# Optimization experiments

Hardware: AMD Instinct MI355X
Metric: run time of the kernel (lower is better)

## Reference

```python
import jax, jax.numpy as jnp
import numpy as np

NUM_NODES = 2_000_000
NUM_PINS = 8_000_000


def setup_inputs() -> dict:
    key = jax.random.key(0)
    k1, k2, k3 = jax.random.split(key, 3)
    # CSR offsets: sorted, pinned to [0, NUM_PINS]
    starts = jnp.sort(jax.random.randint(k1, (NUM_NODES + 1,), 0, NUM_PINS + 1, dtype=jnp.int32))
    starts = starts.at[0].set(0).at[-1].set(NUM_PINS)
    # flat node->pin map: a permutation of all pin ids (each pin belongs to one node)
    flat_node2pin = jax.random.permutation(k2, NUM_PINS).astype(jnp.int32)
    # per-pin sort key (a permutation -> unique keys, like a global pin ordering)
    sorted_pin_map = jax.random.permutation(k3, NUM_PINS).astype(jnp.int32)
    return {
        "flat_node2pin_start": starts,
        "flat_node2pin": flat_node2pin,
        "sorted_pin_map": sorted_pin_map,
        "num_nodes": NUM_NODES,
    }


def reference(flat_node2pin_start, flat_node2pin, sorted_pin_map, num_nodes):
    """For each node, return the pin id (from its CSR segment) with the minimum
    sorted_pin_map value; 0 for nodes with no pins (matching zeros init)."""
    num_pins = flat_node2pin.shape[0]
    pin_pos = jnp.arange(num_pins, dtype=jnp.int32)
    # segment id for each flat pin slot: node i owns [starts[i], starts[i+1])
    seg = (jnp.searchsorted(flat_node2pin_start, pin_pos, side="right") - 1).astype(jnp.int32)
    key = sorted_pin_map[flat_node2pin]  # ordering key per flat slot
    min_key = jax.ops.segment_min(key, seg, num_segments=num_nodes)  # [num_nodes]
    # pick the pin achieving the min key (ties -> smallest pin id, keys unique here)
    cand = jnp.where(key == min_key[seg], flat_node2pin, jnp.int32(num_pins))
    best_pin = jax.ops.segment_min(cand, seg, num_segments=num_nodes)
    counts = flat_node2pin_start[1:] - flat_node2pin_start[:-1]
    node2pinId = jnp.where(counts > 0, best_pin, jnp.int32(0)).astype(jnp.int32)
    return node2pinId
```

## Files before the change

### kernel.cpp

```cpp
#include <hip/hip_runtime.h>
#include <stdint.h>


typedef int iv4 __attribute__((ext_vector_type(4)));

#define NPB 512
#define NT  256
#define CAP 2560
#define PINMASK 0x7FFFFFu

__global__ void build_key4_kernel(const int* __restrict__ key,
                                  uint32_t* __restrict__ key4,
                                  int num_pins, int shift) {
    int t = blockIdx.x * blockDim.x + threadIdx.x;
    int base = t * 8;
    if (base >= num_pins) return;
    if (base + 8 <= num_pins) {
        const iv4* kp = (const iv4*)(key + base);
        iv4 a = __builtin_nontemporal_load(kp);
        iv4 b = __builtin_nontemporal_load(kp + 1);
        uint32_t w = 0;
        w |= (((uint32_t)a.x >> shift) & 15u) << 0;
        w |= (((uint32_t)a.y >> shift) & 15u) << 4;
        w |= (((uint32_t)a.z >> shift) & 15u) << 8;
        w |= (((uint32_t)a.w >> shift) & 15u) << 12;
        w |= (((uint32_t)b.x >> shift) & 15u) << 16;
        w |= (((uint32_t)b.y >> shift) & 15u) << 20;
        w |= (((uint32_t)b.z >> shift) & 15u) << 24;
        w |= (((uint32_t)b.w >> shift) & 15u) << 28;
        __builtin_nontemporal_store(w, key4 + t);
    } else {
        uint32_t w = 0;
        for (int j = 0; base + j < num_pins; ++j) {
            uint32_t k = (uint32_t)key[base + j];
            w |= ((k >> shift) & 15u) << (4 * j);
        }
        __builtin_nontemporal_store(w, key4 + t);
    }
}

__device__ __forceinline__ uint32_t nib_of(const uint32_t* key4, uint32_t p) {
    uint32_t w = key4[p >> 3];
    return (w >> ((p & 7u) * 4u)) & 15u;
}

__device__ __forceinline__ iv4 load_chunk(const int* __restrict__ n2p,
                                          int jal, int jbeg, int jend, int c) {
    int j0 = jal + (c << 2);
    if (j0 >= jbeg && j0 + 4 <= jend) {
        return __builtin_nontemporal_load((const iv4*)(n2p + j0));
    }
    iv4 r;
    #pragma unroll
    for (int e = 0; e < 4; ++e) {
        int j = j0 + e;
        r[e] = (j >= jbeg && j < jend) ? __builtin_nontemporal_load(n2p + j)
                                       : -1;
    }
    return r;
}

__device__ __forceinline__ uint32_t pack_sv(const uint32_t* key4, int pi) {
    if (pi < 0) return 0xFFFFFFFFu;
    uint32_t p = (uint32_t)pi;
    return (nib_of(key4, p) << 23) | p;
}

__device__ __forceinline__ void upd3(uint32_t sp, uint32_t& m1, uint32_t& m2,
                                     uint32_t& m3) {
    uint32_t a = min(sp, m1);
    uint32_t b = max(sp, m1);
    uint32_t c = min(b, m2);
    uint32_t d = max(b, m2);
    m1 = a; m2 = c; m3 = min(d, m3);
}

__device__ __forceinline__ int scan_seg3(const uint32_t* slot, int s, int e,
                                         const int* __restrict__ key) {
    if (e <= s) return 0;
    uint32_t m1 = ~0u, m2 = ~0u, m3 = ~0u;
    for (int q = (s & ~3); q < e; q += 4) {
        iv4 v = *(const iv4*)(slot + q);
        #pragma unroll
        for (int u = 0; u < 4; ++u) {
            int j = q + u;
            uint32_t sp = (uint32_t)v[u];
            sp = (j >= s && j < e) ? sp : ~0u;
            upd3(sp, m1, m2, m3);
        }
    }
    uint32_t nib1 = m1 >> 23;
    if ((m2 >> 23) != nib1) return (int)(m1 & PINMASK);
    if ((m3 >> 23) != nib1) {
        int p1 = (int)(m1 & PINMASK), p2 = (int)(m2 & PINMASK);
        int k1 = key[p1], k2 = key[p2];
        return k1 < k2 ? p1 : p2;
    }
    int bk = 0x7fffffff, r = 0;
    for (int q = s; q < e; ++q) {
        uint32_t sp = slot[q];
        if ((sp >> 23) == nib1) {
            int p = (int)(sp & PINMASK);
            int k = key[p];
            if (k < bk) { bk = k; r = p; }
        }
    }
    return r;
}

__global__ __launch_bounds__(NT) void SortNode2Pin_stage_kernel(
        const int* __restrict__ starts,
        const int* __restrict__ n2p,
        const int* __restrict__ key,
        const uint32_t* __restrict__ key4,
        int* __restrict__ out,
        int num_nodes) {
    __shared__ __align__(16) uint32_t slot[CAP + 8];

    int t = threadIdx.x;
    int i0 = blockIdx.x * NPB;

    int iend = i0 + NPB; if (iend > num_nodes) iend = num_nodes;
    int jbeg0 = starts[i0 < num_nodes ? i0 : num_nodes];
    int jend0 = starts[iend];

    int iA = i0 + t;        if (iA > num_nodes) iA = num_nodes;
    int iA1 = iA + 1;       if (iA1 > num_nodes) iA1 = num_nodes;
    int iB = i0 + NT + t;   if (iB > num_nodes) iB = num_nodes;
    int iB1 = iB + 1;       if (iB1 > num_nodes) iB1 = num_nodes;
    int sA = starts[iA], eA = starts[iA1];
    int sB = starts[iB], eB = starts[iB1];

    int range = jend0 - jbeg0;

    if (range <= CAP) {
        int jal = jbeg0 & ~3;
        int nch = (jend0 - jal + 3) >> 2;
        int c = t;
        for (; c + NT < nch; c += 2 * NT) {
            int c2 = c + NT;
            iv4 pa = load_chunk(n2p, jal, jbeg0, jend0, c);
            iv4 pb = load_chunk(n2p, jal, jbeg0, jend0, c2);
            iv4 wa, wb;
            #pragma unroll
            for (int u = 0; u < 4; ++u) wa[u] = (int)pack_sv(key4, pa[u]);
            #pragma unroll
            for (int u = 0; u < 4; ++u) wb[u] = (int)pack_sv(key4, pb[u]);
            *(iv4*)&slot[c  << 2] = wa;
            *(iv4*)&slot[c2 << 2] = wb;
        }
        for (; c < nch; c += NT) {
            iv4 pa = load_chunk(n2p, jal, jbeg0, jend0, c);
            iv4 wa;
            #pragma unroll
            for (int u = 0; u < 4; ++u) wa[u] = (int)pack_sv(key4, pa[u]);
            *(iv4*)&slot[c << 2] = wa;
        }
        __syncthreads();

        int ra = scan_seg3(slot, sA - jal, eA - jal, key);
        int rb = scan_seg3(slot, sB - jal, eB - jal, key);
        int na = i0 + t;
        int nb = i0 + NT + t;
        if (na < num_nodes) __builtin_nontemporal_store(ra, out + na);
        if (nb < num_nodes) __builtin_nontemporal_store(rb, out + nb);
    } else {
        for (int idx = t; idx < NPB; idx += NT) {
            int node = i0 + idx;
            if (node >= num_nodes) break;
            int s = starts[node], e = starts[node + 1];
            int mv = 16, bp = 0, bk = -1;
            for (int j = s; j < e; ++j) {
                uint32_t p = (uint32_t)n2p[j];
                int n = (int)nib_of(key4, p);
                if (n > mv) continue;
                if (n < mv) { mv = n; bp = (int)p; bk = -1; }
                else {
                    if (bk < 0) bk = key[bp];
                    int k = key[p];
                    if (k < bk) { bk = k; bp = (int)p; }
                }
            }
            __builtin_nontemporal_store(bp, out + node);
        }
    }
}

__global__ void SortNode2Pin_direct_kernel(const int* __restrict__ starts,
                                           const int* __restrict__ n2p,
                                           const int* __restrict__ key,
                                           int* __restrict__ out,
                                           int num_nodes) {
    int i = blockIdx.x * blockDim.x + threadIdx.x;
    if (i >= num_nodes) return;
    int s = starts[i];
    int e = starts[i + 1];
    int best_pin = 0;
    int best_key = 0x7fffffff;
    for (int j = s; j < e; ++j) {
        int p = n2p[j];
        int k = key[p];
        if (k < best_key) { best_key = k; best_pin = p; }
    }
    out[i] = best_pin;
}

extern "C" void kernel_launch(void* const* d_in, const int* in_sizes, int n_in,
                              void* d_out, int out_size, void* d_ws, size_t ws_size,
                              hipStream_t stream) {
    const int* starts = (const int*)d_in[0];
    const int* n2p    = (const int*)d_in[1];
    const int* key    = (const int*)d_in[2];
    int num_nodes = out_size;
    int num_pins  = in_sizes[1];

    size_t key4_words = (size_t)((num_pins + 7) / 8);
    size_t need = key4_words * sizeof(uint32_t);

    if (ws_size >= need && num_pins < (1 << 23)) {
        int bits = 32 - __builtin_clz((unsigned)(num_pins - 1));
        int shift = bits > 4 ? bits - 4 : 0;
        uint32_t* key4 = (uint32_t*)d_ws;

        int g1 = (int)((key4_words + NT - 1) / NT);
        build_key4_kernel<<<g1, NT, 0, stream>>>(key, key4, num_pins, shift);

        int g2 = (num_nodes + NPB - 1) / NPB;
        SortNode2Pin_stage_kernel<<<g2, NT, 0, stream>>>(
            starts, n2p, key, key4, (int*)d_out, num_nodes);
    } else {
        int grid = (num_nodes + 255) / 256;
        SortNode2Pin_direct_kernel<<<grid, 256, 0, stream>>>(
            starts, n2p, key, (int*)d_out, num_nodes);
    }
}
```

Baseline: 82.88 us.

## Process four nodes per thread and batch key lookups to raise memory-level parallelism

Doubles nodes per block to 1024 and enlarges the shared staging buffer, so each thread now handles four node segments instead of two. The fill loop is unrolled to four chunks per iteration, and the final resolution is split into phases so the two-candidate key lookups for all four segments are issued together rather than serially. The aim is more outstanding gathers per thread and fewer blocks, at the cost of more registers, more shared memory per block (lower occupancy), and a larger fallback risk when a block's pin range exceeds the cap.

```diff
diff --git a/kernel.cpp b/kernel.cpp
--- a/kernel.cpp
+++ b/kernel.cpp
@@ -4,9 +4,10 @@
 
 typedef int iv4 __attribute__((ext_vector_type(4)));
 
-#define NPB 512
+#define NPB 1024
 #define NT  256
-#define CAP 2560
+#define SEGS 4
+#define CAP 4608
 #define PINMASK 0x7FFFFFu
 
 __global__ void build_key4_kernel(const int* __restrict__ key,
@@ -75,10 +76,9 @@
     m1 = a; m2 = c; m3 = min(d, m3);
 }
 
-__device__ __forceinline__ int scan_seg3(const uint32_t* slot, int s, int e,
-                                         const int* __restrict__ key) {
-    if (e <= s) return 0;
-    uint32_t m1 = ~0u, m2 = ~0u, m3 = ~0u;
+__device__ __forceinline__ void scan_mins(const uint32_t* slot, int s, int e,
+                                          uint32_t& m1, uint32_t& m2, uint32_t& m3) {
+    m1 = ~0u; m2 = ~0u; m3 = ~0u;
     for (int q = (s & ~3); q < e; q += 4) {
         iv4 v = *(const iv4*)(slot + q);
         #pragma unroll
@@ -89,23 +89,6 @@
             upd3(sp, m1, m2, m3);
         }
     }
-    uint32_t nib1 = m1 >> 23;
-    if ((m2 >> 23) != nib1) return (int)(m1 & PINMASK);
-    if ((m3 >> 23) != nib1) {
-        int p1 = (int)(m1 & PINMASK), p2 = (int)(m2 & PINMASK);
-        int k1 = key[p1], k2 = key[p2];
-        return k1 < k2 ? p1 : p2;
-    }
-    int bk = 0x7fffffff, r = 0;
-    for (int q = s; q < e; ++q) {
-        uint32_t sp = slot[q];
-        if ((sp >> 23) == nib1) {
-            int p = (int)(sp & PINMASK);
-            int k = key[p];
-            if (k < bk) { bk = k; r = p; }
-        }
-    }
-    return r;
 }
 
 __global__ __launch_bounds__(NT) void SortNode2Pin_stage_kernel(
@@ -123,31 +106,39 @@
     int iend = i0 + NPB; if (iend > num_nodes) iend = num_nodes;
     int jbeg0 = starts[i0 < num_nodes ? i0 : num_nodes];
     int jend0 = starts[iend];
-
-    int iA = i0 + t;        if (iA > num_nodes) iA = num_nodes;
-    int iA1 = iA + 1;       if (iA1 > num_nodes) iA1 = num_nodes;
-    int iB = i0 + NT + t;   if (iB > num_nodes) iB = num_nodes;
-    int iB1 = iB + 1;       if (iB1 > num_nodes) iB1 = num_nodes;
-    int sA = starts[iA], eA = starts[iA1];
-    int sB = starts[iB], eB = starts[iB1];
-
     int range = jend0 - jbeg0;
+
+    int sS[SEGS], eS[SEGS];
+    #pragma unroll
+    for (int k = 0; k < SEGS; ++k) {
+        int ia = i0 + k * NT + t;  if (ia > num_nodes) ia = num_nodes;
+        int ib = ia + 1;           if (ib > num_nodes) ib = num_nodes;
+        sS[k] = starts[ia];
+        eS[k] = starts[ib];
+    }
 
     if (range <= CAP) {
         int jal = jbeg0 & ~3;
         int nch = (jend0 - jal + 3) >> 2;
         int c = t;
-        for (; c + NT < nch; c += 2 * NT) {
-            int c2 = c + NT;
-            iv4 pa = load_chunk(n2p, jal, jbeg0, jend0, c);
-            iv4 pb = load_chunk(n2p, jal, jbeg0, jend0, c2);
-            iv4 wa, wb;
-            #pragma unroll
-            for (int u = 0; u < 4; ++u) wa[u] = (int)pack_sv(key4, pa[u]);
-            #pragma unroll
-            for (int u = 0; u < 4; ++u) wb[u] = (int)pack_sv(key4, pb[u]);
-            *(iv4*)&slot[c  << 2] = wa;
-            *(iv4*)&slot[c2 << 2] = wb;
+        for (; c + 3 * NT < nch; c += 4 * NT) {
+            iv4 p0 = load_chunk(n2p, jal, jbeg0, jend0, c);
+            iv4 p1 = load_chunk(n2p, jal, jbeg0, jend0, c + NT);
+            iv4 p2 = load_chunk(n2p, jal, jbeg0, jend0, c + 2 * NT);
+            iv4 p3 = load_chunk(n2p, jal, jbeg0, jend0, c + 3 * NT);
+            iv4 w0, w1, w2, w3;
+            #pragma unroll
+            for (int u = 0; u < 4; ++u) w0[u] = (int)pack_sv(key4, p0[u]);
+            #pragma unroll
+            for (int u = 0; u < 4; ++u) w1[u] = (int)pack_sv(key4, p1[u]);
+            #pragma unroll
+            for (int u = 0; u < 4; ++u) w2[u] = (int)pack_sv(key4, p2[u]);
+            #pragma unroll
+            for (int u = 0; u < 4; ++u) w3[u] = (int)pack_sv(key4, p3[u]);
+            *(iv4*)&slot[(c           ) << 2] = w0;
+            *(iv4*)&slot[(c +     NT  ) << 2] = w1;
+            *(iv4*)&slot[(c + 2 * NT  ) << 2] = w2;
+            *(iv4*)&slot[(c + 3 * NT  ) << 2] = w3;
         }
         for (; c < nch; c += NT) {
             iv4 pa = load_chunk(n2p, jal, jbeg0, jend0, c);
@@ -158,12 +149,66 @@
         }
         __syncthreads();
 
-        int ra = scan_seg3(slot, sA - jal, eA - jal, key);
-        int rb = scan_seg3(slot, sB - jal, eB - jal, key);
-        int na = i0 + t;
-        int nb = i0 + NT + t;
-        if (na < num_nodes) __builtin_nontemporal_store(ra, out + na);
-        if (nb < num_nodes) __builtin_nontemporal_store(rb, out + nb);
+        uint32_t M1[SEGS], M2[SEGS], M3[SEGS];
+        #pragma unroll
+        for (int k = 0; k < SEGS; ++k)
+            scan_mins(slot, sS[k] - jal, eS[k] - jal, M1[k], M2[k], M3[k]);
+
+        int res[SEGS];
+        int pa[SEGS], pb[SEGS];
+        bool two[SEGS], multi[SEGS];
+        #pragma unroll
+        for (int k = 0; k < SEGS; ++k) {
+            two[k] = false; multi[k] = false;
+            pa[k] = 0; pb[k] = 0;
+            uint32_t b1 = M1[k] >> 23;
+            if (eS[k] <= sS[k]) {
+                res[k] = 0;
+            } else if ((M2[k] >> 23) != b1) {
+                res[k] = (int)(M1[k] & PINMASK);
+            } else if ((M3[k] >> 23) != b1) {
+                two[k] = true;
+                pa[k] = (int)(M1[k] & PINMASK);
+                pb[k] = (int)(M2[k] & PINMASK);
+                res[k] = 0;
+            } else {
+                multi[k] = true;
+                res[k] = 0;
+            }
+        }
+        int ka[SEGS], kb[SEGS];
+        #pragma unroll
+        for (int k = 0; k < SEGS; ++k) {
+            ka[k] = 0; kb[k] = 0;
+            if (two[k]) { ka[k] = key[pa[k]]; kb[k] = key[pb[k]]; }
+        }
+        #pragma unroll
+        for (int k = 0; k < SEGS; ++k)
+            if (two[k]) res[k] = ka[k] < kb[k] ? pa[k] : pb[k];
+
+        #pragma unroll
+        for (int k = 0; k < SEGS; ++k) {
+            if (multi[k]) {
+                uint32_t b1 = M1[k] >> 23;
+                int bk = 0x7fffffff, r = 0;
+                for (int q = sS[k] - jal; q < eS[k] - jal; ++q) {
+                    uint32_t sp = slot[q];
+                    if ((sp >> 23) == b1) {
+                        int p = (int)(sp & PINMASK);
+                        int kk = key[p];
+                        if (kk < bk) { bk = kk; r = p; }
+                    }
+                }
+                res[k] = r;
+            }
+        }
+
+        #pragma unroll
+        for (int k = 0; k < SEGS; ++k) {
+            int node = i0 + k * NT + t;
+            if (node < num_nodes)
+                __builtin_nontemporal_store(res[k], out + node);
+        }
     } else {
         for (int idx = t; idx < NPB; idx += NT) {
             int node = i0 + idx;
```

Result: slower. 85.78 us (+3.5%).
